# Optimization experiments

Measured on AMD Instinct MI355X. Metric: run time of the kernel, lower is better.

Reference implementation:

```python
import jax, jax.numpy as jnp
import numpy as np
from jax import lax

K = 3  # local kernel size (k in the module)
PAD = K // 2

def _conv2d(x, w, b, pad):
    # x: [B,Cin,H,W], w: [Cout,Cin,kh,kw]
    y = lax.conv_general_dilated(
        x, w, window_strides=(1, 1), padding=[(pad, pad), (pad, pad)],
        dimension_numbers=('NCHW', 'OIHW', 'NCHW'))
    return y + b[None, :, None, None]

def setup_inputs() -> dict:
    key = jax.random.key(0)
    ks = jax.random.split(key, 4)
    B, C, H, W = 8, 64, 256, 256
    lr_t = jax.random.normal(ks[0], (B, 3, H, W), dtype=jnp.float32)
    h_tm1 = jax.random.normal(ks[1], (B, C, H, W), dtype=jnp.float32)
    w1 = jax.random.normal(ks[2], (C, 3, 3, 3), dtype=jnp.float32) * (1.0 / np.sqrt(3 * 9))
    b1 = jnp.zeros((C,), dtype=jnp.float32)
    w2 = jax.random.normal(ks[3], (K * K, C, 1, 1), dtype=jnp.float32) * (1.0 / np.sqrt(C))
    b2 = jnp.zeros((K * K,), dtype=jnp.float32)
    return {"lr_t": lr_t, "h_tm1": h_tm1, "w1": w1, "b1": b1, "w2": w2, "b2": b2}

def reference(lr_t, h_tm1, w1, b1, w2, b2):
    B, C, H, W = h_tm1.shape
    # k_proj: Conv2d(3,dim,3,p=1) -> ReLU -> Conv2d(dim,k^2,1)
    kern = _conv2d(jax.nn.relu(_conv2d(lr_t, w1, b1, 1)), w2, b2, 0)  # [B,k^2,H,W]
    # Fused unfold * kernel -> sum over k^2 taps, without materializing [B,C,H,W,k^2].
    # F.unfold orders taps row-major: tap index = i*K + j.
    h_pad = jnp.pad(h_tm1, ((0, 0), (0, 0), (PAD, PAD), (PAD, PAD)))
    sim = jnp.zeros_like(h_tm1)
    for i in range(K):
        for j in range(K):
            shifted = lax.dynamic_slice(h_pad, (0, 0, i, j), (B, C, H, W))
            sim = sim + shifted * kern[:, i * K + j][:, None, :, :]
    return h_tm1 * jax.nn.sigmoid(sim)
```

## Files before the change

### kernel.cpp

```cpp
#include <hip/hip_runtime.h>
#include <hip/hip_bf16.h>
#include <math.h>

constexpr int B_  = 8;
constexpr int CIN = 3;
constexpr int C_  = 64;
constexpr int H_  = 256;
constexpr int W_  = 256;
constexpr int TAPS = 9;
constexpr int KROW = TAPS * W_ / 2;

typedef float f32x4 __attribute__((ext_vector_type(4)));
typedef unsigned int u32x2 __attribute__((ext_vector_type(2)));

static __device__ __forceinline__ unsigned short f2bf(float f) {
    unsigned int u = __float_as_uint(f);
    unsigned int r = (u + 0x7fffu + ((u >> 16) & 1u)) >> 16;
    return (unsigned short)r;
}

__global__ __launch_bounds__(256, 4)
void hsa_kern(const float* __restrict__ lr,
              const float* __restrict__ w1,
              const float* __restrict__ b1,
              const float* __restrict__ w2,
              const float* __restrict__ b2,
              unsigned short* __restrict__ kws)
{
    __shared__ float w2t[C_][12];

    const int tid = threadIdx.x;
    const int blk = blockIdx.x;
    const int b = blk / H_;
    const int y = blk % H_;

    for (int i = tid; i < TAPS * C_; i += 256) {
        const int t = i / C_;
        const int c = i % C_;
        w2t[c][t] = w2[i];
    }
    __syncthreads();

    const int x = tid;
    float win[CIN][3][3];
    #pragma unroll
    for (int ci = 0; ci < CIN; ++ci) {
        #pragma unroll
        for (int r = 0; r < 3; ++r) {
            const int yy = y + r - 1;
            const bool vy = (unsigned)yy < (unsigned)H_;
            const float* row = lr + ((size_t)(b * CIN + ci) * H_ + yy) * W_;
            win[ci][r][0] = (vy && x > 0)       ? row[x - 1] : 0.f;
            win[ci][r][1] = vy                   ? row[x]     : 0.f;
            win[ci][r][2] = (vy && x < W_ - 1)  ? row[x + 1] : 0.f;
        }
    }

    float acc[TAPS];
    #pragma unroll
    for (int t = 0; t < TAPS; ++t) acc[t] = b2[t];

    for (int c = 0; c < C_; ++c) {
        const float* wc = w1 + c * 27;
        float h0 = b1[c], h1 = 0.f, h2 = 0.f;
        #pragma unroll
        for (int r = 0; r < 3; ++r)
            #pragma unroll
            for (int j = 0; j < 3; ++j) {
                h0 = fmaf(wc[(0 * 3 + r) * 3 + j], win[0][r][j], h0);
                h1 = fmaf(wc[(1 * 3 + r) * 3 + j], win[1][r][j], h1);
                h2 = fmaf(wc[(2 * 3 + r) * 3 + j], win[2][r][j], h2);
            }
        const float hsum = fmaxf((h0 + h1) + h2, 0.f);

        const float4 wa = *(const float4*)&w2t[c][0];
        const float4 wb = *(const float4*)&w2t[c][4];
        const float  w8 = w2t[c][8];
        acc[0] = fmaf(wa.x, hsum, acc[0]);
        acc[1] = fmaf(wa.y, hsum, acc[1]);
        acc[2] = fmaf(wa.z, hsum, acc[2]);
        acc[3] = fmaf(wa.w, hsum, acc[3]);
        acc[4] = fmaf(wb.x, hsum, acc[4]);
        acc[5] = fmaf(wb.y, hsum, acc[5]);
        acc[6] = fmaf(wb.z, hsum, acc[6]);
        acc[7] = fmaf(wb.w, hsum, acc[7]);
        acc[8] = fmaf(w8,  hsum, acc[8]);
    }

    unsigned short* kr = kws + (size_t)(b * H_ + y) * (TAPS * W_);
    #pragma unroll
    for (int t = 0; t < TAPS; ++t) kr[t * W_ + x] = f2bf(acc[t]);
}

__global__ __launch_bounds__(256, 4)
void hsa_gate(const float* __restrict__ hin,
              const unsigned short* __restrict__ kws,
              float* __restrict__ out)
{
    const int tid = threadIdx.x;
    const int bid = blockIdx.x;
    const int nb  = (bid & 7) * 128 + (bid >> 3);
    const int b     = nb >> 7;
    const int strip = (nb >> 2) & 31;
    const int cg    = nb & 3;
    const int Y     = strip * 8;

    const int lane = tid & 63;
    const int wv   = tid >> 6;
    const int x0   = lane * 4;
    const int c0   = cg * 16 + wv * 4;

    const size_t plane = (size_t)H_ * W_;
    const float* hb = hin + ((size_t)b * C_ + c0) * plane;
    float*       ob = out + ((size_t)b * C_ + c0) * plane;
    const unsigned int* kbase = (const unsigned int*)kws + (size_t)b * H_ * KROW;

    const float lmask = (lane > 0)  ? 1.f : 0.f;
    const float rmask = (lane < 63) ? 1.f : 0.f;

    f32x4 win[3][4];

    {
        const int ym = (Y > 0) ? (Y - 1) : 0;
        #pragma unroll
        for (int i = 0; i < 4; ++i)
            win[0][i] = *(const f32x4*)(hb + i * plane + (size_t)ym      * W_ + x0);
        #pragma unroll
        for (int i = 0; i < 4; ++i)
            win[1][i] = *(const f32x4*)(hb + i * plane + (size_t)Y       * W_ + x0);
        #pragma unroll
        for (int i = 0; i < 4; ++i)
            win[2][i] = *(const f32x4*)(hb + i * plane + (size_t)(Y + 1) * W_ + x0);
    }

    #pragma unroll
    for (int yy = 0; yy < 8; ++yy) {
        const int yg = Y + yy;

        f32x4 kt[TAPS];
        {
            const unsigned int* kr = kbase + (size_t)yg * KROW + lane * 2;
            #pragma unroll
            for (int t = 0; t < TAPS; ++t) {
                const u32x2 w = *(const u32x2*)(kr + t * 128);
                kt[t].x = __uint_as_float(w.x << 16);
                kt[t].y = __uint_as_float(w.x & 0xffff0000u);
                kt[t].z = __uint_as_float(w.y << 16);
                kt[t].w = __uint_as_float(w.y & 0xffff0000u);
            }
        }

        f32x4 nxt[4];
        if (yy < 7) {
            const int yn = (yg + 2 < H_) ? (yg + 2) : (H_ - 1);
            #pragma unroll
            for (int i = 0; i < 4; ++i)
                nxt[i] = *(const f32x4*)(hb + i * plane + (size_t)yn * W_ + x0);
        }

        const float m0 = (yg > 0)      ? 1.f : 0.f;
        const float m2 = (yg < H_ - 1) ? 1.f : 0.f;
        #pragma unroll
        for (int t = 0; t < 3; ++t) { kt[t] *= m0; kt[6 + t] *= m2; }
        kt[0].x *= lmask; kt[3].x *= lmask; kt[6].x *= lmask;
        kt[2].w *= rmask; kt[5].w *= rmask; kt[8].w *= rmask;

        float sim[4][4];
        #pragma unroll
        for (int i = 0; i < 4; ++i)
            #pragma unroll
            for (int j = 0; j < 4; ++j) sim[i][j] = 0.f;

        #pragma unroll
        for (int r = 0; r < 3; ++r) {
            const int sl = (yy + r) % 3;
            const f32x4 k0 = kt[r * 3 + 0];
            const f32x4 k1 = kt[r * 3 + 1];
            const f32x4 k2 = kt[r * 3 + 2];
            #pragma unroll
            for (int i = 0; i < 4; ++i) {
                const f32x4 cv = win[sl][i];
                const float l  = __shfl_up(cv.w, 1);
                const float rr = __shfl_down(cv.x, 1);
                sim[i][0] = fmaf(l,    k0.x, fmaf(cv.x, k1.x, fmaf(cv.y, k2.x, sim[i][0])));
                sim[i][1] = fmaf(cv.x, k0.y, fmaf(cv.y, k1.y, fmaf(cv.z, k2.y, sim[i][1])));
                sim[i][2] = fmaf(cv.y, k0.z, fmaf(cv.z, k1.z, fmaf(cv.w, k2.z, sim[i][2])));
                sim[i][3] = fmaf(cv.z, k0.w, fmaf(cv.w, k1.w, fmaf(rr,   k2.w, sim[i][3])));
            }
        }

        #pragma unroll
        for (int i = 0; i < 4; ++i) {
            const f32x4 ctr = win[(yy + 1) % 3][i];
            f32x4 o;
            o.x = ctr.x * __builtin_amdgcn_rcpf(1.f + __expf(-sim[i][0]));
            o.y = ctr.y * __builtin_amdgcn_rcpf(1.f + __expf(-sim[i][1]));
            o.z = ctr.z * __builtin_amdgcn_rcpf(1.f + __expf(-sim[i][2]));
            o.w = ctr.w * __builtin_amdgcn_rcpf(1.f + __expf(-sim[i][3]));
            __builtin_nontemporal_store(o, (f32x4*)(ob + i * plane + (size_t)yg * W_ + x0));
        }

        if (yy < 7) {
            #pragma unroll
            for (int i = 0; i < 4; ++i) win[yy % 3][i] = nxt[i];
        }
    }
}

__global__ __launch_bounds__(256, 4)
void hsa_fused(const float* __restrict__ lr,
               const float* __restrict__ hin,
               const float* __restrict__ w1,
               const float* __restrict__ b1,
               const float* __restrict__ w2,
               const float* __restrict__ b2,
               float* __restrict__ out)
{
    __shared__ float kernS[TAPS][W_];
    __shared__ float w2t[C_][12];

    const int tid = threadIdx.x;
    const int blk = blockIdx.x;
    const int b = blk / H_;
    const int y = blk % H_;

    for (int i = tid; i < TAPS * C_; i += 256) {
        const int t = i / C_;
        const int c = i % C_;
        w2t[c][t] = w2[i];
    }
    __syncthreads();

    {
        const int x = tid;
        float win[CIN][3][3];
        #pragma unroll
        for (int ci = 0; ci < CIN; ++ci)
            #pragma unroll
            for (int r = 0; r < 3; ++r) {
                const int yy = y + r - 1;
                const bool vy = (unsigned)yy < (unsigned)H_;
                const float* row = lr + ((size_t)(b * CIN + ci) * H_ + yy) * W_;
                win[ci][r][0] = (vy && x > 0)      ? row[x - 1] : 0.f;
                win[ci][r][1] = vy                  ? row[x]     : 0.f;
                win[ci][r][2] = (vy && x < W_ - 1) ? row[x + 1] : 0.f;
            }

        float acc[TAPS];
        #pragma unroll
        for (int t = 0; t < TAPS; ++t) acc[t] = b2[t];

        for (int c = 0; c < C_; ++c) {
            const float* wc = w1 + c * 27;
            float h0 = b1[c], h1 = 0.f, h2 = 0.f;
            #pragma unroll
            for (int r = 0; r < 3; ++r)
                #pragma unroll
                for (int j = 0; j < 3; ++j) {
                    h0 = fmaf(wc[(0 * 3 + r) * 3 + j], win[0][r][j], h0);
                    h1 = fmaf(wc[(1 * 3 + r) * 3 + j], win[1][r][j], h1);
                    h2 = fmaf(wc[(2 * 3 + r) * 3 + j], win[2][r][j], h2);
                }
            const float hsum = fmaxf((h0 + h1) + h2, 0.f);
            const float4 wa = *(const float4*)&w2t[c][0];
            const float4 wb = *(const float4*)&w2t[c][4];
            const float  w8 = w2t[c][8];
            acc[0] = fmaf(wa.x, hsum, acc[0]);
            acc[1] = fmaf(wa.y, hsum, acc[1]);
            acc[2] = fmaf(wa.z, hsum, acc[2]);
            acc[3] = fmaf(wa.w, hsum, acc[3]);
            acc[4] = fmaf(wb.x, hsum, acc[4]);
            acc[5] = fmaf(wb.y, hsum, acc[5]);
            acc[6] = fmaf(wb.z, hsum, acc[6]);
            acc[7] = fmaf(wb.w, hsum, acc[7]);
            acc[8] = fmaf(w8,  hsum, acc[8]);
        }
        #pragma unroll
        for (int t = 0; t < TAPS; ++t) kernS[t][x] = acc[t];
    }
    __syncthreads();

    const int lane = tid & 63;
    const int wav  = tid >> 6;
    const int x0   = lane * 4;

    float4 kt[TAPS];
    #pragma unroll
    for (int t = 0; t < TAPS; ++t) kt[t] = *(const float4*)&kernS[t][x0];

    #pragma unroll 4
    for (int cc = 0; cc < 16; ++cc) {
        const int c = wav * 16 + cc;
        const float* hb = hin + (size_t)(b * C_ + c) * H_ * W_;

        float4 rowv[3];
        float  lft[3], rgt[3];
        #pragma unroll
        for (int r = 0; r < 3; ++r) {
            const int yy = y + r - 1;
            const bool vy = (unsigned)yy < (unsigned)H_;
            float4 m;
            if (vy) m = *(const float4*)(hb + (size_t)yy * W_ + x0);
            else    m = make_float4(0.f, 0.f, 0.f, 0.f);
            rowv[r] = m;
            float l  = __shfl_up(m.w, 1);
            float rr = __shfl_down(m.x, 1);
            if (lane == 0)  l  = 0.f;
            if (lane == 63) rr = 0.f;
            lft[r] = l; rgt[r] = rr;
        }

        float sim0 = 0.f, sim1 = 0.f, sim2 = 0.f, sim3 = 0.f;
        #pragma unroll
        for (int r = 0; r < 3; ++r) {
            const float w6_0 = lft[r];
            const float w6_1 = rowv[r].x;
            const float w6_2 = rowv[r].y;
            const float w6_3 = rowv[r].z;
            const float w6_4 = rowv[r].w;
            const float w6_5 = rgt[r];
            { const float4 k4 = kt[r*3+0];
              sim0 = fmaf(w6_0, k4.x, sim0); sim1 = fmaf(w6_1, k4.y, sim1);
              sim2 = fmaf(w6_2, k4.z, sim2); sim3 = fmaf(w6_3, k4.w, sim3); }
            { const float4 k4 = kt[r*3+1];
              sim0 = fmaf(w6_1, k4.x, sim0); sim1 = fmaf(w6_2, k4.y, sim1);
              sim2 = fmaf(w6_3, k4.z, sim2); sim3 = fmaf(w6_4, k4.w, sim3); }
            { const float4 k4 = kt[r*3+2];
              sim0 = fmaf(w6_2, k4.x, sim0); sim1 = fmaf(w6_3, k4.y, sim1);
              sim2 = fmaf(w6_4, k4.z, sim2); sim3 = fmaf(w6_5, k4.w, sim3); }
        }

        float4 o;
        o.x = rowv[1].x * __builtin_amdgcn_rcpf(1.f + __expf(-sim0));
        o.y = rowv[1].y * __builtin_amdgcn_rcpf(1.f + __expf(-sim1));
        o.z = rowv[1].z * __builtin_amdgcn_rcpf(1.f + __expf(-sim2));
        o.w = rowv[1].w * __builtin_amdgcn_rcpf(1.f + __expf(-sim3));
        *(float4*)(out + ((size_t)(b * C_ + c) * H_ + y) * W_ + x0) = o;
    }
}

extern "C" void kernel_launch(void* const* d_in, const int* in_sizes, int n_in,
                              void* d_out, int out_size, void* d_ws, size_t ws_size,
                              hipStream_t stream) {
    const float* lr  = (const float*)d_in[0];
    const float* hin = (const float*)d_in[1];
    const float* w1  = (const float*)d_in[2];
    const float* b1  = (const float*)d_in[3];
    const float* w2  = (const float*)d_in[4];
    const float* b2  = (const float*)d_in[5];
    float* out = (float*)d_out;

    const size_t kern_bytes = (size_t)B_ * H_ * TAPS * W_ * sizeof(unsigned short);

    if (ws_size >= kern_bytes) {
        unsigned short* kws = (unsigned short*)d_ws;
        hipLaunchKernelGGL(hsa_kern, dim3(B_ * H_), dim3(256), 0, stream,
                           lr, w1, b1, w2, b2, kws);
        hipLaunchKernelGGL(hsa_gate, dim3(1024), dim3(256), 0, stream,
                           hin, kws, out);
    } else {
        hipLaunchKernelGGL(hsa_fused, dim3(B_ * H_), dim3(256), 0, stream,
                           lr, hin, w1, b1, w2, b2, out);
    }
}
```

Measured before the change: 89.39 us.

## Split gate kernel to one channel per wave and stage tap weights in LDS

Each wave in the gate kernel now handles one channel instead of four, and the grid grows from 1024 to 4096 blocks, which cuts per-thread register use and raises occupancy. The bf16 tap weights for the block's 8-row strip are loaded once into shared memory (about 36 KB) and read from there, instead of every wave reading them from global memory. The trade-off is that kernel weights are now fetched from global memory by four times as many blocks, and the large LDS allocation may cap how many blocks fit per CU.

```diff
diff --git a/kernel.cpp b/kernel.cpp
--- a/kernel.cpp
+++ b/kernel.cpp
@@ -12,6 +12,7 @@
 
 typedef float f32x4 __attribute__((ext_vector_type(4)));
 typedef unsigned int u32x2 __attribute__((ext_vector_type(2)));
+typedef unsigned int u32x4 __attribute__((ext_vector_type(4)));
 
 static __device__ __forceinline__ unsigned short f2bf(float f) {
     unsigned int u = __float_as_uint(f);
@@ -97,18 +98,20 @@
               const unsigned short* __restrict__ kws,
               float* __restrict__ out)
 {
+    __shared__ unsigned int ksh[8][KROW];
+
     const int tid = threadIdx.x;
     const int bid = blockIdx.x;
-    const int nb  = (bid & 7) * 128 + (bid >> 3);
-    const int b     = nb >> 7;
-    const int strip = (nb >> 2) & 31;
-    const int cg    = nb & 3;
+    const int nb  = (bid & 7) * 512 + (bid >> 3);
+    const int b     = nb >> 9;
+    const int strip = (nb >> 4) & 31;
+    const int cg    = nb & 15;
     const int Y     = strip * 8;
 
     const int lane = tid & 63;
     const int wv   = tid >> 6;
     const int x0   = lane * 4;
-    const int c0   = cg * 16 + wv * 4;
+    const int c0   = cg * 4 + wv;
 
     const size_t plane = (size_t)H_ * W_;
     const float* hb = hin + ((size_t)b * C_ + c0) * plane;
@@ -118,44 +121,43 @@
     const float lmask = (lane > 0)  ? 1.f : 0.f;
     const float rmask = (lane < 63) ? 1.f : 0.f;
 
-    f32x4 win[3][4];
-
+    {
+        const unsigned int* kr = kbase + (size_t)Y * KROW;
+        unsigned int* ksf = &ksh[0][0];
+        #pragma unroll
+        for (int i = 0; i < 9; ++i) {
+            const int idx = (tid + i * 256) * 4;
+            *(u32x4*)(ksf + idx) = *(const u32x4*)(kr + idx);
+        }
+    }
+
+    f32x4 wA, wB, wC;
     {
         const int ym = (Y > 0) ? (Y - 1) : 0;
-        #pragma unroll
-        for (int i = 0; i < 4; ++i)
-            win[0][i] = *(const f32x4*)(hb + i * plane + (size_t)ym      * W_ + x0);
-        #pragma unroll
-        for (int i = 0; i < 4; ++i)
-            win[1][i] = *(const f32x4*)(hb + i * plane + (size_t)Y       * W_ + x0);
-        #pragma unroll
-        for (int i = 0; i < 4; ++i)
-            win[2][i] = *(const f32x4*)(hb + i * plane + (size_t)(Y + 1) * W_ + x0);
-    }
+        wA = *(const f32x4*)(hb + (size_t)ym      * W_ + x0);
+        wB = *(const f32x4*)(hb + (size_t)Y       * W_ + x0);
+        wC = *(const f32x4*)(hb + (size_t)(Y + 1) * W_ + x0);
+    }
+    __syncthreads();
 
     #pragma unroll
     for (int yy = 0; yy < 8; ++yy) {
         const int yg = Y + yy;
 
-        f32x4 kt[TAPS];
-        {
-            const unsigned int* kr = kbase + (size_t)yg * KROW + lane * 2;
-            #pragma unroll
-            for (int t = 0; t < TAPS; ++t) {
-                const u32x2 w = *(const u32x2*)(kr + t * 128);
-                kt[t].x = __uint_as_float(w.x << 16);
-                kt[t].y = __uint_as_float(w.x & 0xffff0000u);
-                kt[t].z = __uint_as_float(w.y << 16);
-                kt[t].w = __uint_as_float(w.y & 0xffff0000u);
-            }
-        }
-
-        f32x4 nxt[4];
+        f32x4 nxt;
         if (yy < 7) {
             const int yn = (yg + 2 < H_) ? (yg + 2) : (H_ - 1);
-            #pragma unroll
-            for (int i = 0; i < 4; ++i)
-                nxt[i] = *(const f32x4*)(hb + i * plane + (size_t)yn * W_ + x0);
+            nxt = *(const f32x4*)(hb + (size_t)yn * W_ + x0);
+        }
+
+        f32x4 kt[TAPS];
+        #pragma unroll
+        for (int t = 0; t < TAPS; ++t) {
+            const u32x2 w = *(const u32x2*)&ksh[yy][t * 128 + lane * 2];
+            kt[t].x = __uint_as_float(w.x << 16);
+            kt[t].y = __uint_as_float(w.x & 0xffff0000u);
+            kt[t].z = __uint_as_float(w.y << 16);
+            kt[t].w = __uint_as_float(w.y & 0xffff0000u);
         }
 
         const float m0 = (yg > 0)      ? 1.f : 0.f;
@@ -165,45 +167,29 @@
         kt[0].x *= lmask; kt[3].x *= lmask; kt[6].x *= lmask;
         kt[2].w *= rmask; kt[5].w *= rmask; kt[8].w *= rmask;
 
-        float sim[4][4];
-        #pragma unroll
-        for (int i = 0; i < 4; ++i)
-            #pragma unroll
-            for (int j = 0; j < 4; ++j) sim[i][j] = 0.f;
-
+        float sim0 = 0.f, sim1 = 0.f, sim2 = 0.f, sim3 = 0.f;
         #pragma unroll
         for (int r = 0; r < 3; ++r) {
-            const int sl = (yy + r) % 3;
+            const f32x4 cv = (r == 0) ? wA : (r == 1) ? wB : wC;
+            const float l  = __shfl_up(cv.w, 1);
+            const float rr = __shfl_down(cv.x, 1);
             const f32x4 k0 = kt[r * 3 + 0];
             const f32x4 k1 = kt[r * 3 + 1];
             const f32x4 k2 = kt[r * 3 + 2];
-            #pragma unroll
-            for (int i = 0; i < 4; ++i) {
-                const f32x4 cv = win[sl][i];
-                const float l  = __shfl_up(cv.w, 1);
-                const float rr = __shfl_down(cv.x, 1);
-                sim[i][0] = fmaf(l,    k0.x, fmaf(cv.x, k1.x, fmaf(cv.y, k2.x, sim[i][0])));
-                sim[i][1] = fmaf(cv.x, k0.y, fmaf(cv.y, k1.y, fmaf(cv.z, k2.y, sim[i][1])));
-                sim[i][2] = fmaf(cv.y, k0.z, fmaf(cv.z, k1.z, fmaf(cv.w, k2.z, sim[i][2])));
-                sim[i][3] = fmaf(cv.z, k0.w, fmaf(cv.w, k1.w, fmaf(rr,   k2.w, sim[i][3])));
-            }
-        }
-
-        #pragma unroll
-        for (int i = 0; i < 4; ++i) {
-            const f32x4 ctr = win[(yy + 1) % 3][i];
-            f32x4 o;
-            o.x = ctr.x * __builtin_amdgcn_rcpf(1.f + __expf(-sim[i][0]));
-            o.y = ctr.y * __builtin_amdgcn_rcpf(1.f + __expf(-sim[i][1]));
-            o.z = ctr.z * __builtin_amdgcn_rcpf(1.f + __expf(-sim[i][2]));
-            o.w = ctr.w * __builtin_amdgcn_rcpf(1.f + __expf(-sim[i][3]));
-            __builtin_nontemporal_store(o, (f32x4*)(ob + i * plane + (size_t)yg * W_ + x0));
-        }
-
-        if (yy < 7) {
-            #pragma unroll
-            for (int i = 0; i < 4; ++i) win[yy % 3][i] = nxt[i];
-        }
+            sim0 = fmaf(l,    k0.x, fmaf(cv.x, k1.x, fmaf(cv.y, k2.x, sim0)));
+            sim1 = fmaf(cv.x, k0.y, fmaf(cv.y, k1.y, fmaf(cv.z, k2.y, sim1)));
+            sim2 = fmaf(cv.y, k0.z, fmaf(cv.z, k1.z, fmaf(cv.w, k2.z, sim2)));
+            sim3 = fmaf(cv.z, k0.w, fmaf(cv.w, k1.w, fmaf(rr,   k2.w, sim3)));
+        }
+
+        f32x4 o;
+        o.x = wB.x * __builtin_amdgcn_rcpf(1.f + __expf(-sim0));
+        o.y = wB.y * __builtin_amdgcn_rcpf(1.f + __expf(-sim1));
+        o.z = wB.z * __builtin_amdgcn_rcpf(1.f + __expf(-sim2));
+        o.w = wB.w * __builtin_amdgcn_rcpf(1.f + __expf(-sim3));
+        __builtin_nontemporal_store(o, (f32x4*)(ob + (size_t)yg * W_ + x0));
+
+        if (yy < 7) { wA = wB; wB = wC; wC = nxt; }
     }
 }
 
@@ -356,7 +342,7 @@
         unsigned short* kws = (unsigned short*)d_ws;
         hipLaunchKernelGGL(hsa_kern, dim3(B_ * H_), dim3(256), 0, stream,
                            lr, w1, b1, w2, b2, kws);
-        hipLaunchKernelGGL(hsa_gate, dim3(1024), dim3(256), 0, stream,
+        hipLaunchKernelGGL(hsa_gate, dim3(4096), dim3(256), 0, stream,
                            hin, kws, out);
     } else {
         hipLaunchKernelGGL(hsa_fused, dim3(B_ * H_), dim3(256), 0, stream,
```

New measurement: 82.83 us, median of 3. -7.3%, faster.
